# Kernel tuning notes

Measured on AMD Instinct MI355X. Metric: run time of the kernel, lower is better.

The kernel has to match this reference:

```python
import jax, jax.numpy as jnp
import numpy as np
import math

D_MODEL = 768
N_HEADS = 12
HEAD_DIM = D_MODEL // N_HEADS
B, T = 2, 4096


def setup_inputs() -> dict:
    key = jax.random.key(0)
    k1, k2, k3, k4 = jax.random.split(key, 4)
    x = jax.random.normal(k1, (B, T, D_MODEL), dtype=jnp.float32)
    mask = jax.random.randint(k2, (B, T), 0, 2).astype(jnp.bool_)
    # torch Linear init scale ~ 1/sqrt(fan_in); use scaled normal for stability
    w_qkv = jax.random.normal(k3, (3 * D_MODEL, D_MODEL), dtype=jnp.float32) / math.sqrt(D_MODEL)
    w_proj = jax.random.normal(k4, (D_MODEL, D_MODEL), dtype=jnp.float32) / math.sqrt(D_MODEL)
    b_proj = jnp.zeros((D_MODEL,), dtype=jnp.float32)
    return {"x": x, "mask": mask, "w_qkv": w_qkv, "w_proj": w_proj, "b_proj": b_proj}


def reference(x, mask, w_qkv, w_proj, b_proj):
    Bb, Tt, D = x.shape
    H, Hd = N_HEADS, HEAD_DIM
    scale = math.sqrt(Hd)
    # qkv projection (bias-free): (B,T,3D) -> (3,B,H,T,Hd)
    qkv = jnp.einsum('btd,ed->bte', x, w_qkv)
    qkv = qkv.reshape(Bb, Tt, 3, H, Hd).transpose(2, 0, 3, 1, 4)
    q, k, v = qkv[0], qkv[1], qkv[2]
    # full T x T scores (faithful to non-fused original)
    attn = jnp.einsum('bhqd,bhkd->bhqk', q, k) / scale
    attn = jnp.where(mask[:, None, None, :], -jnp.inf, attn)
    attn = jax.nn.softmax(attn, axis=-1)  # dropout p=0 -> identity
    out = jnp.einsum('bhqk,bhkd->bhqd', attn, v)
    out = out.transpose(0, 2, 1, 3).reshape(Bb, Tt, D)
    return jnp.einsum('btd,ed->bte', out, w_proj) + b_proj
```

## Files before the change

kernel.cpp:

```cpp
#include <hip/hip_runtime.h>

#define D_MODEL 768
#define N_HEADS 12
#define SEQ 4096
#define KVB 64

typedef __attribute__((ext_vector_type(4))) float f32x4;
typedef __attribute__((ext_vector_type(16))) float f32x16;
typedef __attribute__((ext_vector_type(8))) short bf16x8;
typedef __attribute__((ext_vector_type(4))) unsigned short u16x4;

typedef __attribute__((address_space(3))) void lds_void;
typedef __attribute__((address_space(1))) const void glb_void;

static __device__ __forceinline__ void gld_lds16(const void* g, void* l) {
    __builtin_amdgcn_global_load_lds((glb_void*)g, (lds_void*)l, 16, 0, 0);
}

static __device__ __forceinline__ unsigned short f32_bf16(float f) {
    union { float f; unsigned int u; } c; c.f = f;
    unsigned int u = c.u;
    u += 0x7FFFu + ((u >> 16) & 1u);
    return (unsigned short)(u >> 16);
}

static __device__ __forceinline__ unsigned int cvtpk(float lo, float hi) {
    unsigned int r;
    asm("v_cvt_pk_bf16_f32 %0, %1, %2" : "=v"(r) : "v"(lo), "v"(hi));
    return r;
}

__global__ void cvt_bf16(const float* __restrict__ in, unsigned short* __restrict__ out, int n) {
    int i = (blockIdx.x * blockDim.x + threadIdx.x) * 4;
    int stride = gridDim.x * blockDim.x * 4;
    for (; i < n; i += stride) {
        f32x4 v = *(const f32x4*)(in + i);
        u16x4 o;
        o[0] = f32_bf16(v[0]); o[1] = f32_bf16(v[1]);
        o[2] = f32_bf16(v[2]); o[3] = f32_bf16(v[3]);
        *(u16x4*)(out + i) = o;
    }
}

__global__ __launch_bounds__(256) void qkv_gemm(const unsigned short* __restrict__ A,
                                                const unsigned short* __restrict__ Bw,
                                                unsigned short* __restrict__ qb,
                                                unsigned short* __restrict__ kb,
                                                unsigned short* __restrict__ vb) {
    __shared__ __attribute__((aligned(16))) unsigned short lA[128*32];
    __shared__ __attribute__((aligned(16))) unsigned short lB[128*32];
    const int K = 768;
    int tid = threadIdx.x;
    int wave = tid >> 6, lane = tid & 63;
    int qr = (wave >> 1) * 64, qc = (wave & 1) * 64;
    int m0 = blockIdx.x * 128, n0 = blockIdx.y * 128;
    f32x4 acc[4][4] = {};
    int c0 = tid * 2;

    for (int kt = 0; kt < K; kt += 32) {
        __syncthreads();
        #pragma unroll
        for (int i = 0; i < 2; ++i) {
            int c = c0 + i;
            int row = c >> 2, col = (c & 3) * 8;
            *(bf16x8*)&lA[row*32 + col] = *(const bf16x8*)(A  + (size_t)(m0 + row) * K + kt + col);
            *(bf16x8*)&lB[row*32 + col] = *(const bf16x8*)(Bw + (size_t)(n0 + row) * K + kt + col);
        }
        __syncthreads();
        bf16x8 af[4], bfr[4];
        #pragma unroll
        for (int m = 0; m < 4; ++m)
            af[m] = *(bf16x8*)&lA[(qr + m*16 + (lane & 15))*32 + (lane >> 4)*8];
        #pragma unroll
        for (int n = 0; n < 4; ++n)
            bfr[n] = *(bf16x8*)&lB[(qc + n*16 + (lane & 15))*32 + (lane >> 4)*8];
        #pragma unroll
        for (int m = 0; m < 4; ++m)
            #pragma unroll
            for (int n = 0; n < 4; ++n)
                acc[m][n] = __builtin_amdgcn_mfma_f32_16x16x32_bf16(af[m], bfr[n], acc[m][n], 0, 0, 0);
    }
    #pragma unroll
    for (int n = 0; n < 4; ++n) {
        int colg = n0 + qc + n*16 + (lane & 15);
        int s = colg / 768;
        int rem = colg - s * 768;
        int h = rem >> 6, d = rem & 63;
        if (s == 2) {
            #pragma unroll
            for (int m = 0; m < 4; ++m) {
                int rowb = m0 + qr + m*16 + (lane >> 4)*4;
                int bb = rowb >> 12, t0 = rowb & 4095;
                u16x4 pk;
                #pragma unroll
                for (int r = 0; r < 4; ++r) pk[r] = f32_bf16(acc[m][n][r]);
                *(u16x4*)(vb + ((size_t)((bb*12 + h)*64 + d))*4096 + t0) = pk;
            }
        } else {
            unsigned short* dst = (s == 0) ? qb : kb;
            float scl = (s == 0) ? 0.125f : 1.0f;
            #pragma unroll
            for (int m = 0; m < 4; ++m) {
                int rowb = m0 + qr + m*16 + (lane >> 4)*4;
                #pragma unroll
                for (int r = 0; r < 4; ++r) {
                    int row = rowb + r;
                    int bb = row >> 12, t = row & 4095;
                    dst[((size_t)((bb*12 + h)*4096 + t))*64 + d] = f32_bf16(acc[m][n][r] * scl);
                }
            }
        }
    }
}

__global__ __launch_bounds__(512, 4) void attn_kern(const unsigned short* __restrict__ qbuf,
                                                    const unsigned short* __restrict__ kbuf,
                                                    const unsigned short* __restrict__ vtbuf,
                                                    const int* __restrict__ mask,
                                                    unsigned short* __restrict__ ob) {
    __shared__ __attribute__((aligned(16))) char lds[2][16384];
    __shared__ float lds_l[4][32];

    const int tid = threadIdx.x, wave = tid >> 6, lane = tid & 63;
    const int l31 = lane & 31, hi2 = lane >> 5;
    const int lane16 = lane * 16;
    const int wq = wave & 3, wk = wave >> 2;

    int raw = blockIdx.x;
    int sb = (raw & 7) * 96 + (raw >> 3);
    int bh = sb >> 5, qi = sb & 31;
    int q0 = qi * 128;
    int b = bh / 12, h = bh - b*12;

    const unsigned short* Qb = qbuf + (size_t)bh * SEQ * 64;
    const unsigned short* Kb = kbuf + (size_t)bh * SEQ * 64;
    const unsigned short* Vt = vtbuf + (size_t)bh * 64 * SEQ;
    const int* mrow = mask + b * SEQ;

    bf16x8 bq[4];
    #pragma unroll
    for (int ds = 0; ds < 4; ++ds)
        bq[ds] = *(const bf16x8*)(Qb + (size_t)(q0 + wq*32 + l31)*64 + ds*16 + hi2*8);

    union U4 { unsigned int w[4]; bf16x8 v; };
    U4 bext; bext.w[0] = (hi2 == 0) ? 0x3F80u : 0u; bext.w[1] = bext.w[2] = bext.w[3] = 0u;

    auto stage = [&](char* buf, int kv0) {
        #pragma unroll
        for (int i = 0; i < 2; ++i) {
            int fi = wave*2 + i;
            const unsigned short* gsrc;
            if (fi < 8) {
                int kt = fi >> 2, ds = fi & 3;
                gsrc = Kb + (size_t)(kv0 + kt*32 + l31)*64 + ds*16 + hi2*8;
            } else {
                int g = fi - 8, dt = g >> 2, ks = g & 3;
                gsrc = Vt + (size_t)(dt*32 + l31)*4096 + kv0 + ks*16 + hi2*8;
            }
            gld_lds16(gsrc, buf + fi*1024);
        }
    };

    f32x16 oacc0 = {}, oacc1 = {};
    float lr = 0.0f;

    stage(lds[0], 0);
    int mb = mrow[wk*32 + l31];
    __syncthreads();

    const int NT = SEQ / KVB;
    for (int t = 0; t < NT; ++t) {
        int kv0 = t * KVB;
        char* bufK = lds[t & 1];
        char* bufV = bufK + 8192;
        int mbn = 0;
        if (t + 1 < NT) {
            stage(lds[(t + 1) & 1], kv0 + KVB);
            mbn = mrow[kv0 + KVB + wk*32 + l31];
        }

        U4 ab;
        ab.w[0] = (hi2 == 0) ? (mb ? 0xC6EAu : 0xC140u) : 0u;
        ab.w[1] = ab.w[2] = ab.w[3] = 0u;

        f32x16 s = {};
        s = __builtin_amdgcn_mfma_f32_32x32x16_bf16(ab.v, bext.v, s, 0, 0, 0);
        #pragma unroll
        for (int ds = 0; ds < 4; ++ds) {
            bf16x8 aK = *(bf16x8*)(bufK + (wk*4 + ds)*1024 + lane16);
            s = __builtin_amdgcn_mfma_f32_32x32x16_bf16(aK, bq[ds], s, 0, 0, 0);
        }

        float rs = 0.0f;
        #pragma unroll
        for (int i = 0; i < 16; ++i) { s[i] = __expf(s[i]); rs += s[i]; }
        rs += __shfl_xor(rs, 32);
        lr += rs;

        bool ishi = (hi2 != 0);
        bf16x8 pa[2];
        #pragma unroll
        for (int sb2 = 0; sb2 < 2; ++sb2) {
            unsigned int X0 = cvtpk(s[8*sb2+0], s[8*sb2+1]);
            unsigned int X1 = cvtpk(s[8*sb2+2], s[8*sb2+3]);
            unsigned int Y0 = cvtpk(s[8*sb2+4], s[8*sb2+5]);
            unsigned int Y1 = cvtpk(s[8*sb2+6], s[8*sb2+7]);
            unsigned int s0 = ishi ? X0 : Y0, s1 = ishi ? X1 : Y1;
            unsigned int r0 = __shfl_xor(s0, 32), r1 = __shfl_xor(s1, 32);
            U4 w;
            w.w[0] = ishi ? r0 : X0;
            w.w[1] = ishi ? r1 : X1;
            w.w[2] = ishi ? Y0 : r0;
            w.w[3] = ishi ? Y1 : r1;
            pa[sb2] = w.v;
        }

        #pragma unroll
        for (int sb2 = 0; sb2 < 2; ++sb2) {
            int ksg = wk*2 + sb2;
            bf16x8 bv0 = *(bf16x8*)(bufV + (0*4 + ksg)*1024 + lane16);
            bf16x8 bv1 = *(bf16x8*)(bufV + (1*4 + ksg)*1024 + lane16);
            oacc0 = __builtin_amdgcn_mfma_f32_32x32x16_bf16(pa[sb2], bv0, oacc0, 0, 0, 0);
            oacc1 = __builtin_amdgcn_mfma_f32_32x32x16_bf16(pa[sb2], bv1, oacc1, 0, 0, 0);
        }

        __syncthreads();
        mb = mbn;
    }

    float* cbase = (float*)lds + wq * 2048;
    if (wk == 1) {
        #pragma unroll
        for (int i = 0; i < 16; ++i) {
            cbase[i*64 + lane]        = oacc0[i];
            cbase[(16 + i)*64 + lane] = oacc1[i];
        }
        if (lane < 32) lds_l[wq][lane] = lr;
    }
    __syncthreads();
    if (wk == 0 && lane < 32) lds_l[wq][lane] += lr;
    __syncthreads();
    if (wk == 0) {
        #pragma unroll
        for (int r = 0; r < 16; ++r) {
            int q = (r & 3) + 8*(r >> 2) + 4*hi2;
            float inv = 1.0f / lds_l[wq][q];
            int tg = q0 + wq*32 + q;
            size_t base = ((size_t)(b*SEQ + tg)) * D_MODEL + h*64 + l31;
            ob[base]      = f32_bf16((oacc0[r] + cbase[r*64 + lane])        * inv);
            ob[base + 32] = f32_bf16((oacc1[r] + cbase[(16 + r)*64 + lane]) * inv);
        }
    }
}

__global__ __launch_bounds__(256) void proj_gemm(const unsigned short* __restrict__ A,
                                                 const unsigned short* __restrict__ Bw,
                                                 const float* __restrict__ bias,
                                                 float* __restrict__ out) {
    __shared__ __attribute__((aligned(16))) unsigned short lA[128*32];
    __shared__ __attribute__((aligned(16))) unsigned short lB[128*32];
    const int K = 768;
    int tid = threadIdx.x;
    int wave = tid >> 6, lane = tid & 63;
    int qr = (wave >> 1) * 64, qc = (wave & 1) * 64;
    int m0 = blockIdx.x * 128, n0 = blockIdx.y * 128;
    f32x4 acc[4][4] = {};
    int c0 = tid * 2;

    for (int kt = 0; kt < K; kt += 32) {
        __syncthreads();
        #pragma unroll
        for (int i = 0; i < 2; ++i) {
            int c = c0 + i;
            int row = c >> 2, col = (c & 3) * 8;
            *(bf16x8*)&lA[row*32 + col] = *(const bf16x8*)(A  + (size_t)(m0 + row) * K + kt + col);
            *(bf16x8*)&lB[row*32 + col] = *(const bf16x8*)(Bw + (size_t)(n0 + row) * K + kt + col);
        }
        __syncthreads();
        bf16x8 af[4], bfr[4];
        #pragma unroll
        for (int m = 0; m < 4; ++m)
            af[m] = *(bf16x8*)&lA[(qr + m*16 + (lane & 15))*32 + (lane >> 4)*8];
        #pragma unroll
        for (int n = 0; n < 4; ++n)
            bfr[n] = *(bf16x8*)&lB[(qc + n*16 + (lane & 15))*32 + (lane >> 4)*8];
        #pragma unroll
        for (int m = 0; m < 4; ++m)
            #pragma unroll
            for (int n = 0; n < 4; ++n)
                acc[m][n] = __builtin_amdgcn_mfma_f32_16x16x32_bf16(af[m], bfr[n], acc[m][n], 0, 0, 0);
    }
    #pragma unroll
    for (int n = 0; n < 4; ++n) {
        int colg = n0 + qc + n*16 + (lane & 15);
        float bn = bias[colg];
        #pragma unroll
        for (int m = 0; m < 4; ++m) {
            int rowb = m0 + qr + m*16 + (lane >> 4)*4;
            #pragma unroll
            for (int r = 0; r < 4; ++r)
                out[(size_t)(rowb + r) * 768 + colg] = acc[m][n][r] + bn;
        }
    }
}

extern "C" void kernel_launch(void* const* d_in, const int* in_sizes, int n_in,
                              void* d_out, int out_size, void* d_ws, size_t ws_size,
                              hipStream_t stream) {
    const float* x      = (const float*)d_in[0];
    const int*   mask   = (const int*)d_in[1];
    const float* w_qkv  = (const float*)d_in[2];
    const float* w_proj = (const float*)d_in[3];
    const float* b_proj = (const float*)d_in[4];
    float* out = (float*)d_out;

    unsigned short* ws = (unsigned short*)d_ws;
    unsigned short* xb     = ws;
    unsigned short* wqkvb  = xb     + 6291456;
    unsigned short* wprojb = wqkvb  + 1769472;
    unsigned short* qb     = wprojb + 589824;
    unsigned short* kb     = qb     + 6291456;
    unsigned short* vtb    = kb     + 6291456;
    unsigned short* ob     = vtb    + 6291456;

    cvt_bf16<<<1024, 256, 0, stream>>>(x,      xb,     6291456);
    cvt_bf16<<<256,  256, 0, stream>>>(w_qkv,  wqkvb,  1769472);
    cvt_bf16<<<128,  256, 0, stream>>>(w_proj, wprojb, 589824);

    qkv_gemm<<<dim3(64, 18), 256, 0, stream>>>(xb, wqkvb, qb, kb, vtb);
    attn_kern<<<768, 512, 0, stream>>>(qb, kb, vtb, mask, ob);
    proj_gemm<<<dim3(64, 6), 256, 0, stream>>>(ob, wprojb, b_proj, out);
}
```

Baseline: 260.0 us.

## Halve attention block waves with two Q tiles per wave, exp2 softmax, swizzled async GEMM loads

```diff
diff --git a/kernel.cpp b/kernel.cpp
--- a/kernel.cpp
+++ b/kernel.cpp
@@ -41,6 +41,8 @@
         *(u16x4*)(out + i) = o;
     }
 }
+
+#define QSCL 0.18033688f
 
 __global__ __launch_bounds__(256) void qkv_gemm(const unsigned short* __restrict__ A,
                                                 const unsigned short* __restrict__ Bw,
@@ -55,25 +57,28 @@
     int qr = (wave >> 1) * 64, qc = (wave & 1) * 64;
     int m0 = blockIdx.x * 128, n0 = blockIdx.y * 128;
     f32x4 acc[4][4] = {};
-    int c0 = tid * 2;
+    const int sl = (((lane >> 4) ^ (lane & 3)) * 16);
 
     for (int kt = 0; kt < K; kt += 32) {
         __syncthreads();
         #pragma unroll
         for (int i = 0; i < 2; ++i) {
-            int c = c0 + i;
-            int row = c >> 2, col = (c & 3) * 8;
-            *(bf16x8*)&lA[row*32 + col] = *(const bf16x8*)(A  + (size_t)(m0 + row) * K + kt + col);
-            *(bf16x8*)&lB[row*32 + col] = *(const bf16x8*)(Bw + (size_t)(n0 + row) * K + kt + col);
+            int c = i*256 + tid;
+            int row = c >> 2;
+            int col = ((c & 3) ^ (row & 3)) * 8;
+            char* dA = (char*)lA + (i*256 + wave*64)*16;
+            char* dB = (char*)lB + (i*256 + wave*64)*16;
+            gld_lds16(A  + (size_t)(m0 + row) * K + kt + col, dA);
+            gld_lds16(Bw + (size_t)(n0 + row) * K + kt + col, dB);
         }
         __syncthreads();
         bf16x8 af[4], bfr[4];
         #pragma unroll
         for (int m = 0; m < 4; ++m)
-            af[m] = *(bf16x8*)&lA[(qr + m*16 + (lane & 15))*32 + (lane >> 4)*8];
+            af[m] = *(bf16x8*)((char*)lA + (qr + m*16 + (lane & 15))*64 + sl);
         #pragma unroll
         for (int n = 0; n < 4; ++n)
-            bfr[n] = *(bf16x8*)&lB[(qc + n*16 + (lane & 15))*32 + (lane >> 4)*8];
+            bfr[n] = *(bf16x8*)((char*)lB + (qc + n*16 + (lane & 15))*64 + sl);
         #pragma unroll
         for (int m = 0; m < 4; ++m)
             #pragma unroll
@@ -98,7 +103,7 @@
             }
         } else {
             unsigned short* dst = (s == 0) ? qb : kb;
-            float scl = (s == 0) ? 0.125f : 1.0f;
+            float scl = (s == 0) ? QSCL : 1.0f;
             #pragma unroll
             for (int m = 0; m < 4; ++m) {
                 int rowb = m0 + qr + m*16 + (lane >> 4)*4;
@@ -113,18 +118,18 @@
     }
 }
 
-__global__ __launch_bounds__(512, 4) void attn_kern(const unsigned short* __restrict__ qbuf,
+__global__ __launch_bounds__(256, 3) void attn_kern(const unsigned short* __restrict__ qbuf,
                                                     const unsigned short* __restrict__ kbuf,
                                                     const unsigned short* __restrict__ vtbuf,
                                                     const int* __restrict__ mask,
                                                     unsigned short* __restrict__ ob) {
     __shared__ __attribute__((aligned(16))) char lds[2][16384];
-    __shared__ float lds_l[4][32];
+    __shared__ float lds_l[2][2][32];
 
     const int tid = threadIdx.x, wave = tid >> 6, lane = tid & 63;
     const int l31 = lane & 31, hi2 = lane >> 5;
     const int lane16 = lane * 16;
-    const int wq = wave & 3, wk = wave >> 2;
+    const int wq = wave & 1, wk = wave >> 1;
 
     int raw = blockIdx.x;
     int sb = (raw & 7) * 96 + (raw >> 3);
@@ -135,120 +140,174 @@
     const unsigned short* Qb = qbuf + (size_t)bh * SEQ * 64;
     const unsigned short* Kb = kbuf + (size_t)bh * SEQ * 64;
     const unsigned short* Vt = vtbuf + (size_t)bh * 64 * SEQ;
-    const int* mrow = mask + b * SEQ;
-
-    bf16x8 bq[4];
+    const int* mrow = mask + b * SEQ + wk*32 + l31;
+
+    bf16x8 bqA[4], bqB[4];
     #pragma unroll
-    for (int ds = 0; ds < 4; ++ds)
-        bq[ds] = *(const bf16x8*)(Qb + (size_t)(q0 + wq*32 + l31)*64 + ds*16 + hi2*8);
+    for (int ds = 0; ds < 4; ++ds) {
+        bqA[ds] = *(const bf16x8*)(Qb + (size_t)(q0 + wq*64 + l31)*64      + ds*16 + hi2*8);
+        bqB[ds] = *(const bf16x8*)(Qb + (size_t)(q0 + wq*64 + 32 + l31)*64 + ds*16 + hi2*8);
+    }
 
     union U4 { unsigned int w[4]; bf16x8 v; };
     U4 bext; bext.w[0] = (hi2 == 0) ? 0x3F80u : 0u; bext.w[1] = bext.w[2] = bext.w[3] = 0u;
 
-    auto stage = [&](char* buf, int kv0) {
-        #pragma unroll
-        for (int i = 0; i < 2; ++i) {
-            int fi = wave*2 + i;
-            const unsigned short* gsrc;
-            if (fi < 8) {
-                int kt = fi >> 2, ds = fi & 3;
-                gsrc = Kb + (size_t)(kv0 + kt*32 + l31)*64 + ds*16 + hi2*8;
-            } else {
-                int g = fi - 8, dt = g >> 2, ks = g & 3;
-                gsrc = Vt + (size_t)(dt*32 + l31)*4096 + kv0 + ks*16 + hi2*8;
-            }
-            gld_lds16(gsrc, buf + fi*1024);
-        }
-    };
-
-    f32x16 oacc0 = {}, oacc1 = {};
-    float lr = 0.0f;
-
-    stage(lds[0], 0);
-    int mb = mrow[wk*32 + l31];
+    const unsigned short* gp[4];
+    ptrdiff_t gstride;
+    if (wave < 2) {
+        #pragma unroll
+        for (int i = 0; i < 4; ++i)
+            gp[i] = Kb + (size_t)(wave*32 + l31)*64 + i*16 + hi2*8;
+        gstride = (ptrdiff_t)KVB * 64;
+    } else {
+        #pragma unroll
+        for (int i = 0; i < 4; ++i)
+            gp[i] = Vt + (size_t)((wave - 2)*32 + l31)*4096 + i*16 + hi2*8;
+        gstride = KVB;
+    }
+
+    f32x16 oA0 = {}, oA1 = {}, oB0 = {}, oB1 = {};
+    float lrA = 0.0f, lrB = 0.0f;
+
+    #pragma unroll
+    for (int i = 0; i < 4; ++i) {
+        gld_lds16(gp[i], lds[0] + (wave*4 + i)*1024);
+        gp[i] += gstride;
+    }
+    int mb = mrow[0];
     __syncthreads();
 
     const int NT = SEQ / KVB;
     for (int t = 0; t < NT; ++t) {
-        int kv0 = t * KVB;
         char* bufK = lds[t & 1];
         char* bufV = bufK + 8192;
         int mbn = 0;
         if (t + 1 < NT) {
-            stage(lds[(t + 1) & 1], kv0 + KVB);
-            mbn = mrow[kv0 + KVB + wk*32 + l31];
+            char* nbuf = lds[(t + 1) & 1];
+            #pragma unroll
+            for (int i = 0; i < 4; ++i) {
+                gld_lds16(gp[i], nbuf + (wave*4 + i)*1024);
+                gp[i] += gstride;
+            }
+            mbn = mrow[(t + 1) * KVB];
         }
 
         U4 ab;
-        ab.w[0] = (hi2 == 0) ? (mb ? 0xC6EAu : 0xC140u) : 0u;
+        ab.w[0] = (hi2 == 0) ? (mb ? 0xC480u : 0xC18Au) : 0u;
         ab.w[1] = ab.w[2] = ab.w[3] = 0u;
 
-        f32x16 s = {};
-        s = __builtin_amdgcn_mfma_f32_32x32x16_bf16(ab.v, bext.v, s, 0, 0, 0);
+        bf16x8 kf[4];
+        #pragma unroll
+        for (int ds = 0; ds < 4; ++ds)
+            kf[ds] = *(bf16x8*)(bufK + (wk*4 + ds)*1024 + lane16);
+
+        __builtin_amdgcn_s_setprio(1);
+        f32x16 sA = {}, sB = {};
+        sA = __builtin_amdgcn_mfma_f32_32x32x16_bf16(ab.v, bext.v, sA, 0, 0, 0);
+        sB = __builtin_amdgcn_mfma_f32_32x32x16_bf16(ab.v, bext.v, sB, 0, 0, 0);
         #pragma unroll
         for (int ds = 0; ds < 4; ++ds) {
-            bf16x8 aK = *(bf16x8*)(bufK + (wk*4 + ds)*1024 + lane16);
-            s = __builtin_amdgcn_mfma_f32_32x32x16_bf16(aK, bq[ds], s, 0, 0, 0);
-        }
-
-        float rs = 0.0f;
-        #pragma unroll
-        for (int i = 0; i < 16; ++i) { s[i] = __expf(s[i]); rs += s[i]; }
-        rs += __shfl_xor(rs, 32);
-        lr += rs;
+            sA = __builtin_amdgcn_mfma_f32_32x32x16_bf16(kf[ds], bqA[ds], sA, 0, 0, 0);
+            sB = __builtin_amdgcn_mfma_f32_32x32x16_bf16(kf[ds], bqB[ds], sB, 0, 0, 0);
+        }
+        __builtin_amdgcn_s_setprio(0);
 
         bool ishi = (hi2 != 0);
-        bf16x8 pa[2];
-        #pragma unroll
-        for (int sb2 = 0; sb2 < 2; ++sb2) {
-            unsigned int X0 = cvtpk(s[8*sb2+0], s[8*sb2+1]);
-            unsigned int X1 = cvtpk(s[8*sb2+2], s[8*sb2+3]);
-            unsigned int Y0 = cvtpk(s[8*sb2+4], s[8*sb2+5]);
-            unsigned int Y1 = cvtpk(s[8*sb2+6], s[8*sb2+7]);
-            unsigned int s0 = ishi ? X0 : Y0, s1 = ishi ? X1 : Y1;
-            unsigned int r0 = __shfl_xor(s0, 32), r1 = __shfl_xor(s1, 32);
+
+        float rsA = 0.0f;
+        #pragma unroll
+        for (int i = 0; i < 16; ++i) { sA[i] = exp2f(sA[i]); rsA += sA[i]; }
+        rsA += __shfl_xor(rsA, 32);
+        lrA += rsA;
+        bf16x8 paA[2];
+        #pragma unroll
+        for (int s2 = 0; s2 < 2; ++s2) {
+            unsigned int X0 = cvtpk(sA[8*s2+0], sA[8*s2+1]);
+            unsigned int X1 = cvtpk(sA[8*s2+2], sA[8*s2+3]);
+            unsigned int Y0 = cvtpk(sA[8*s2+4], sA[8*s2+5]);
+            unsigned int Y1 = cvtpk(sA[8*s2+6], sA[8*s2+7]);
+            unsigned int a0 = ishi ? X0 : Y0, a1 = ishi ? X1 : Y1;
+            unsigned int r0 = __shfl_xor(a0, 32), r1 = __shfl_xor(a1, 32);
             U4 w;
             w.w[0] = ishi ? r0 : X0;
             w.w[1] = ishi ? r1 : X1;
             w.w[2] = ishi ? Y0 : r0;
             w.w[3] = ishi ? Y1 : r1;
-            pa[sb2] = w.v;
-        }
-
-        #pragma unroll
-        for (int sb2 = 0; sb2 < 2; ++sb2) {
-            int ksg = wk*2 + sb2;
-            bf16x8 bv0 = *(bf16x8*)(bufV + (0*4 + ksg)*1024 + lane16);
-            bf16x8 bv1 = *(bf16x8*)(bufV + (1*4 + ksg)*1024 + lane16);
-            oacc0 = __builtin_amdgcn_mfma_f32_32x32x16_bf16(pa[sb2], bv0, oacc0, 0, 0, 0);
-            oacc1 = __builtin_amdgcn_mfma_f32_32x32x16_bf16(pa[sb2], bv1, oacc1, 0, 0, 0);
-        }
+            paA[s2] = w.v;
+        }
+        __builtin_amdgcn_s_setprio(1);
+        #pragma unroll
+        for (int s2 = 0; s2 < 2; ++s2) {
+            int ksg = wk*2 + s2;
+            bf16x8 bv0 = *(bf16x8*)(bufV + (    ksg)*1024 + lane16);
+            bf16x8 bv1 = *(bf16x8*)(bufV + (4 + ksg)*1024 + lane16);
+            oA0 = __builtin_amdgcn_mfma_f32_32x32x16_bf16(paA[s2], bv0, oA0, 0, 0, 0);
+            oA1 = __builtin_amdgcn_mfma_f32_32x32x16_bf16(paA[s2], bv1, oA1, 0, 0, 0);
+        }
+        __builtin_amdgcn_s_setprio(0);
+
+        float rsB = 0.0f;
+        #pragma unroll
+        for (int i = 0; i < 16; ++i) { sB[i] = exp2f(sB[i]); rsB += sB[i]; }
+        rsB += __shfl_xor(rsB, 32);
+        lrB += rsB;
+        bf16x8 paB[2];
+        #pragma unroll
+        for (int s2 = 0; s2 < 2; ++s2) {
+            unsigned int X0 = cvtpk(sB[8*s2+0], sB[8*s2+1]);
+            unsigned int X1 = cvtpk(sB[8*s2+2], sB[8*s2+3]);
+            unsigned int Y0 = cvtpk(sB[8*s2+4], sB[8*s2+5]);
+            unsigned int Y1 = cvtpk(sB[8*s2+6], sB[8*s2+7]);
+            unsigned int a0 = ishi ? X0 : Y0, a1 = ishi ? X1 : Y1;
+            unsigned int r0 = __shfl_xor(a0, 32), r1 = __shfl_xor(a1, 32);
+            U4 w;
+            w.w[0] = ishi ? r0 : X0;
+            w.w[1] = ishi ? r1 : X1;
+            w.w[2] = ishi ? Y0 : r0;
+            w.w[3] = ishi ? Y1 : r1;
+            paB[s2] = w.v;
+        }
+        __builtin_amdgcn_s_setprio(1);
+        #pragma unroll
+        for (int s2 = 0; s2 < 2; ++s2) {
+            int ksg = wk*2 + s2;
+            bf16x8 bv0 = *(bf16x8*)(bufV + (    ksg)*1024 + lane16);
+            bf16x8 bv1 = *(bf16x8*)(bufV + (4 + ksg)*1024 + lane16);
+            oB0 = __builtin_amdgcn_mfma_f32_32x32x16_bf16(paB[s2], bv0, oB0, 0, 0, 0);
+            oB1 = __builtin_amdgcn_mfma_f32_32x32x16_bf16(paB[s2], bv1, oB1, 0, 0, 0);
+        }
+        __builtin_amdgcn_s_setprio(0);
 
         __syncthreads();
         mb = mbn;
     }
 
-    float* cbase = (float*)lds + wq * 2048;
+    float* cbase = (float*)lds + wq * 4096;
     if (wk == 1) {
         #pragma unroll
         for (int i = 0; i < 16; ++i) {
-            cbase[i*64 + lane]        = oacc0[i];
-            cbase[(16 + i)*64 + lane] = oacc1[i];
-        }
-        if (lane < 32) lds_l[wq][lane] = lr;
-    }
-    __syncthreads();
-    if (wk == 0 && lane < 32) lds_l[wq][lane] += lr;
+            cbase[(     i)*64 + lane] = oA0[i];
+            cbase[(16 + i)*64 + lane] = oA1[i];
+            cbase[(32 + i)*64 + lane] = oB0[i];
+            cbase[(48 + i)*64 + lane] = oB1[i];
+        }
+        if (lane < 32) { lds_l[wq][0][lane] = lrA; lds_l[wq][1][lane] = lrB; }
+    }
     __syncthreads();
     if (wk == 0) {
+        if (lane < 32) { lds_l[wq][0][lane] += lrA; lds_l[wq][1][lane] += lrB; }
         #pragma unroll
         for (int r = 0; r < 16; ++r) {
             int q = (r & 3) + 8*(r >> 2) + 4*hi2;
-            float inv = 1.0f / lds_l[wq][q];
-            int tg = q0 + wq*32 + q;
-            size_t base = ((size_t)(b*SEQ + tg)) * D_MODEL + h*64 + l31;
-            ob[base]      = f32_bf16((oacc0[r] + cbase[r*64 + lane])        * inv);
-            ob[base + 32] = f32_bf16((oacc1[r] + cbase[(16 + r)*64 + lane]) * inv);
+            float invA = 1.0f / lds_l[wq][0][q];
+            float invB = 1.0f / lds_l[wq][1][q];
+            int tA = q0 + wq*64 + q;
+            size_t baseA = ((size_t)(b*SEQ + tA)) * D_MODEL + h*64 + l31;
+            size_t baseB = baseA + (size_t)32 * D_MODEL;
+            ob[baseA]      = f32_bf16((oA0[r] + cbase[(     r)*64 + lane]) * invA);
+            ob[baseA + 32] = f32_bf16((oA1[r] + cbase[(16 + r)*64 + lane]) * invA);
+            ob[baseB]      = f32_bf16((oB0[r] + cbase[(32 + r)*64 + lane]) * invB);
+            ob[baseB + 32] = f32_bf16((oB1[r] + cbase[(48 + r)*64 + lane]) * invB);
         }
     }
 }
@@ -265,25 +324,28 @@
     int qr = (wave >> 1) * 64, qc = (wave & 1) * 64;
     int m0 = blockIdx.x * 128, n0 = blockIdx.y * 128;
     f32x4 acc[4][4] = {};
-    int c0 = tid * 2;
+    const int sl = (((lane >> 4) ^ (lane & 3)) * 16);
 
     for (int kt = 0; kt < K; kt += 32) {
         __syncthreads();
         #pragma unroll
         for (int i = 0; i < 2; ++i) {
-            int c = c0 + i;
-            int row = c >> 2, col = (c & 3) * 8;
-            *(bf16x8*)&lA[row*32 + col] = *(const bf16x8*)(A  + (size_t)(m0 + row) * K + kt + col);
-            *(bf16x8*)&lB[row*32 + col] = *(const bf16x8*)(Bw + (size_t)(n0 + row) * K + kt + col);
+            int c = i*256 + tid;
+            int row = c >> 2;
+            int col = ((c & 3) ^ (row & 3)) * 8;
+            char* dA = (char*)lA + (i*256 + wave*64)*16;
+            char* dB = (char*)lB + (i*256 + wave*64)*16;
+            gld_lds16(A  + (size_t)(m0 + row) * K + kt + col, dA);
+            gld_lds16(Bw + (size_t)(n0 + row) * K + kt + col, dB);
         }
         __syncthreads();
         bf16x8 af[4], bfr[4];
         #pragma unroll
         for (int m = 0; m < 4; ++m)
-            af[m] = *(bf16x8*)&lA[(qr + m*16 + (lane & 15))*32 + (lane >> 4)*8];
+            af[m] = *(bf16x8*)((char*)lA + (qr + m*16 + (lane & 15))*64 + sl);
         #pragma unroll
         for (int n = 0; n < 4; ++n)
-            bfr[n] = *(bf16x8*)&lB[(qc + n*16 + (lane & 15))*32 + (lane >> 4)*8];
+            bfr[n] = *(bf16x8*)((char*)lB + (qc + n*16 + (lane & 15))*64 + sl);
         #pragma unroll
         for (int m = 0; m < 4; ++m)
             #pragma unroll
@@ -328,6 +390,6 @@
     cvt_bf16<<<128,  256, 0, stream>>>(w_proj, wprojb, 589824);
 
     qkv_gemm<<<dim3(64, 18), 256, 0, stream>>>(xb, wqkvb, qb, kb, vtb);
-    attn_kern<<<768, 512, 0, stream>>>(qb, kb, vtb, mask, ob);
+    attn_kern<<<768, 256, 0, stream>>>(qb, kb, vtb, mask, ob);
     proj_gemm<<<dim3(64, 6), 256, 0, stream>>>(ob, wprojb, b_proj, out);
 }
```

After: 544.0 us. 109% more time.
